# Kernel optimization log

Measured on AMD Instinct MI355X. Metric: run time of the kernel, lower is better.

## Reference

```python
import jax, jax.numpy as jnp
import numpy as np

N = 50000
E = 800000
D = 128
NEG_SLOPE = 0.2


def _gat_layer(x, W, al, ar, b, src, dst):
    """Single-head DGL-style GATConv with ReLU activation."""
    z = x @ W                                    # [N, D] projected features
    el = z @ al                                  # [N] left attention logits
    er = z @ ar                                  # [N] right attention logits
    e = jax.nn.leaky_relu(el[src] + er[dst], NEG_SLOPE)   # [E]
    # softmax over incoming edges per destination node (numerically stable)
    m = jax.ops.segment_max(e, dst, num_segments=N)       # [N]
    ex = jnp.exp(e - m[dst])                               # [E]
    s = jax.ops.segment_sum(ex, dst, num_segments=N)       # [N]
    alpha = ex / s[dst]                                    # [E]
    out = jax.ops.segment_sum(alpha[:, None] * z[src], dst, num_segments=N)  # [N, D]
    return jax.nn.relu(out + b)


def setup_inputs() -> dict:
    key = jax.random.key(0)
    ks = jax.random.split(key, 16)
    s = 0.05
    inp = {
        "f": jax.random.normal(ks[0], (N, D), dtype=jnp.float32),
        "src": jax.random.randint(ks[1], (E,), 0, N, dtype=jnp.int32),
        "dst": jax.random.randint(ks[2], (E,), 0, N, dtype=jnp.int32),
    }
    for i, kb in zip((1, 2, 3), (3, 7, 11)):
        inp[f"W{i}"] = jax.random.normal(ks[kb], (D, D), dtype=jnp.float32) * s
        inp[f"al{i}"] = jax.random.normal(ks[kb + 1], (D,), dtype=jnp.float32) * s
        inp[f"ar{i}"] = jax.random.normal(ks[kb + 2], (D,), dtype=jnp.float32) * s
        inp[f"b{i}"] = jnp.zeros((D,), dtype=jnp.float32)
    return inp


def reference(f, src, dst, W1, al1, ar1, b1, W2, al2, ar2, b2, W3, al3, ar3, b3):
    h = _gat_layer(f, W1, al1, ar1, b1, src, dst)
    h = _gat_layer(h, W2, al2, ar2, b2, src, dst)
    h = _gat_layer(h, W3, al3, ar3, b3, src, dst)
    return h  # [N, D] (single head already squeezed)
```

## Files before the change

kernel.cpp:

```cpp
#include <hip/hip_runtime.h>
#include <hip/hip_fp16.h>
#include <math.h>

#define NN 50000
#define NE 800000
#define DD 128
#define NEG_SLOPE 0.2f
#define CAP 64
#define GBLK ((NN + 127) / 128)
#define WSBLK (3 * 16384 / 256)
#define HBLK ((NE + 255) / 256)
#define SBLK ((NE + 511) / 512)

typedef short frag8 __attribute__((ext_vector_type(8)));
typedef float f32x4 __attribute__((ext_vector_type(4)));

__device__ __forceinline__ unsigned bf16_rne(float x) {
  unsigned u = __float_as_uint(x);
  return (u + 0x7FFFu + ((u >> 16) & 1u)) >> 16;
}

__device__ __forceinline__ void wsplit_body(
    int bid, const float* __restrict__ W0, const float* __restrict__ W1,
    const float* __restrict__ W2, short* __restrict__ Wh, short* __restrict__ Wl) {
  int gidx = bid * 256 + threadIdx.x;
  int L = gidx >> 14;
  int idx = gidx & 16383;
  const float* W = (L == 0) ? W0 : (L == 1) ? W1 : W2;
  int j = idx & 7;
  int lane = (idx >> 3) & 63;
  int tile = idx >> 9;
  int nt = tile & 7, kt = tile >> 3;
  int k = kt * 32 + (lane >> 4) * 8 + j;
  int n = nt * 16 + (lane & 15);
  float x = W[k * DD + n];
  unsigned hu = bf16_rne(x);
  float hf = __uint_as_float(hu << 16);
  unsigned lu = bf16_rne(x - hf);
  Wh[gidx] = (short)hu;
  Wl[gidx] = (short)lu;
}

__device__ __forceinline__ void hist_body(int bid, const int* __restrict__ dst,
                                          int* __restrict__ deg,
                                          unsigned short* __restrict__ edge_slot) {
  int i = bid * 256 + threadIdx.x;
  if (i < NE) edge_slot[i] = (unsigned short)atomicAdd(&deg[dst[i]], 1);
}

__global__ __launch_bounds__(256) void fused_pre(
    const float* __restrict__ W0, const float* __restrict__ W1, const float* __restrict__ W2,
    short* __restrict__ Wh, short* __restrict__ Wl,
    const int* __restrict__ dst, int* __restrict__ deg,
    unsigned short* __restrict__ edge_slot) {
  if (blockIdx.x < WSBLK) wsplit_body(blockIdx.x, W0, W1, W2, Wh, Wl);
  else hist_body(blockIdx.x - WSBLK, dst, deg, edge_slot);
}

__device__ __forceinline__ void gemm_body(
    int bid, short (*sB)[8192],
    const float* __restrict__ x, const short* __restrict__ Wh, const short* __restrict__ Wl,
    const float* __restrict__ al, const float* __restrict__ ar,
    __half* __restrict__ z, float* __restrict__ el, float* __restrict__ er) {
  const int t = threadIdx.x;
  const int w = t >> 6, lane = t & 63;
  const int m = lane & 15, quad = lane >> 4;
  const int R0 = bid * 128 + w * 16;

  auto stage = [&](int kt, int buf) {
    const uint4* gh = (const uint4*)(Wh + kt * 4096);
    const uint4* gl = (const uint4*)(Wl + kt * 4096);
    uint4* s = (uint4*)sB[buf];
    s[t] = gh[t];
    s[t + 512] = gl[t];
  };

  f32x4 acc[8];
#pragma unroll
  for (int nt = 0; nt < 8; nt++) acc[nt] = (f32x4)(0.f);

  int rA = R0 + m; if (rA > NN - 1) rA = NN - 1;

  stage(0, 0);
  __syncthreads();

#pragma unroll
  for (int kt = 0; kt < 4; kt++) {
    const int buf = kt & 1;
    if (kt < 3) stage(kt + 1, buf ^ 1);

    const float* xp = x + (size_t)rA * DD + kt * 32 + quad * 8;
    float xv[8];
    *(float4*)(xv) = *(const float4*)xp;
    *(float4*)(xv + 4) = *(const float4*)(xp + 4);
    frag8 ah, alo;
#pragma unroll
    for (int j = 0; j < 8; j++) {
      unsigned hu = bf16_rne(xv[j]);
      float hf = __uint_as_float(hu << 16);
      ah[j] = (short)hu;
      alo[j] = (short)bf16_rne(xv[j] - hf);
    }
#pragma unroll
    for (int nt = 0; nt < 8; nt++) {
      frag8 bh = *(const frag8*)&sB[buf][nt * 512 + lane * 8];
      frag8 bl = *(const frag8*)&sB[buf][4096 + nt * 512 + lane * 8];
      acc[nt] = __builtin_amdgcn_mfma_f32_16x16x32_bf16(alo, bh, acc[nt], 0, 0, 0);
      acc[nt] = __builtin_amdgcn_mfma_f32_16x16x32_bf16(ah, bl, acc[nt], 0, 0, 0);
      acc[nt] = __builtin_amdgcn_mfma_f32_16x16x32_bf16(ah, bh, acc[nt], 0, 0, 0);
    }
    __syncthreads();
  }

  float alv[8], arv[8];
#pragma unroll
  for (int nt = 0; nt < 8; nt++) { alv[nt] = al[nt * 16 + m]; arv[nt] = ar[nt * 16 + m]; }
#pragma unroll
  for (int r = 0; r < 4; r++) {
    float pl = 0.f, pr = 0.f;
#pragma unroll
    for (int nt = 0; nt < 8; nt++) { pl += acc[nt][r] * alv[nt]; pr += acc[nt][r] * arv[nt]; }
#pragma unroll
    for (int off = 8; off; off >>= 1) {
      pl += __shfl_xor(pl, off, 64);
      pr += __shfl_xor(pr, off, 64);
    }
    int row = R0 + quad * 4 + r;
    if (row < NN) {
      if (m == 0) { el[row] = pl; er[row] = pr; }
#pragma unroll
      for (int nt = 0; nt < 8; nt++) {
        unsigned short hu = __half_as_ushort(__float2half(acc[nt][r]));
        unsigned short hn = (unsigned short)__shfl_xor((int)hu, 1, 64);
        if ((m & 1) == 0) {
          __half2 pair = __halves2half2(__ushort_as_half(hu), __ushort_as_half(hn));
          *(__half2*)(z + (size_t)row * DD + nt * 16 + m) = pair;
        }
      }
    }
  }
}

__device__ __forceinline__ void scatter_body(
    int bid, const int* __restrict__ src, const int* __restrict__ dst,
    const unsigned short* __restrict__ edge_slot, unsigned short* __restrict__ csr_src) {
  int i = bid * 512 + threadIdx.x;
  if (i >= NE) return;
  int slot = edge_slot[i]; if (slot > CAP - 1) slot = CAP - 1;
  csr_src[dst[i] * CAP + slot] = (unsigned short)src[i];
}

__global__ __launch_bounds__(512) void gemm_mfma(
    const float* __restrict__ x, const short* __restrict__ Wh, const short* __restrict__ Wl,
    const float* __restrict__ al, const float* __restrict__ ar,
    __half* __restrict__ z, float* __restrict__ el, float* __restrict__ er) {
  __shared__ __align__(16) short sB[2][8192];
  gemm_body(blockIdx.x, sB, x, Wh, Wl, al, ar, z, el, er);
}

__global__ __launch_bounds__(512) void fused_scatter_gemm(
    const float* __restrict__ x, const short* __restrict__ Wh, const short* __restrict__ Wl,
    const float* __restrict__ al, const float* __restrict__ ar,
    __half* __restrict__ z, float* __restrict__ el, float* __restrict__ er,
    const int* __restrict__ src, const int* __restrict__ dst,
    const unsigned short* __restrict__ edge_slot, unsigned short* __restrict__ csr_src) {
  __shared__ __align__(16) short sB[2][8192];
  if (blockIdx.x < GBLK) gemm_body(blockIdx.x, sB, x, Wh, Wl, al, ar, z, el, er);
  else scatter_body(blockIdx.x - GBLK, src, dst, edge_slot, csr_src);
}

__global__ __launch_bounds__(256) void gat_agg(
    const int* __restrict__ deg, const unsigned short* __restrict__ csr_src,
    const float* __restrict__ el, const float* __restrict__ er,
    const __half* __restrict__ z, const float* __restrict__ b,
    float* __restrict__ out) {
  int node = (int)((blockIdx.x * 256 + threadIdx.x) >> 6);
  int lane = threadIdx.x & 63;
  if (node >= NN) return;
  int dn = deg[node]; if (dn > CAP) dn = CAP;
  int beg = node * CAP, end = beg + dn;
  float erd = er[node];
  const __half2* zb = (const __half2*)z + lane;

  float2 acc = make_float2(0.f, 0.f);
  float ssum = 0.f;
  for (int base = beg; base < end; base += 64) {
    int j = base + lane;
    int sn = 0; float w = 0.f;
    if (j < end) {
      sn = csr_src[j];
      float e = el[sn] + erd;
      e = (e > 0.f) ? e : NEG_SLOPE * e;
      w = __expf(e);
    }
    ssum += w;
    int cnt = min(64, end - base);
    int jj = 0;
    for (; jj + 8 <= cnt; jj += 8) {
      float ww[8]; int ss[8];
#pragma unroll
      for (int u = 0; u < 8; u++) {
        ww[u] = __shfl(w, jj + u, 64);
        ss[u] = __shfl(sn, jj + u, 64);
      }
      float2 zv[8];
#pragma unroll
      for (int u = 0; u < 8; u++) zv[u] = __half22float2(zb[(size_t)ss[u] * 64]);
#pragma unroll
      for (int u = 0; u < 8; u++) { acc.x += ww[u] * zv[u].x; acc.y += ww[u] * zv[u].y; }
    }
    for (; jj < cnt; jj++) {
      float wj = __shfl(w, jj, 64);
      int snj = __shfl(sn, jj, 64);
      float2 zv = __half22float2(zb[(size_t)snj * 64]);
      acc.x += wj * zv.x; acc.y += wj * zv.y;
    }
  }
#pragma unroll
  for (int off = 32; off; off >>= 1) ssum += __shfl_xor(ssum, off, 64);
  float inv_s = (dn > 0) ? 1.f / ssum : 0.f;

  float2 bv = *(const float2*)(b + lane * 2);
  float ox = fmaxf(acc.x * inv_s + bv.x, 0.f);
  float oy = fmaxf(acc.y * inv_s + bv.y, 0.f);
  *(float2*)(out + (size_t)node * DD + lane * 2) = make_float2(ox, oy);
}

extern "C" void kernel_launch(void* const* d_in, const int* in_sizes, int n_in,
                              void* d_out, int out_size, void* d_ws, size_t ws_size,
                              hipStream_t stream) {
  const float* f   = (const float*)d_in[0];
  const int*   src = (const int*)d_in[1];
  const int*   dst = (const int*)d_in[2];
  const float* W[3]  = {(const float*)d_in[3], (const float*)d_in[7],  (const float*)d_in[11]};
  const float* al[3] = {(const float*)d_in[4], (const float*)d_in[8],  (const float*)d_in[12]};
  const float* ar[3] = {(const float*)d_in[5], (const float*)d_in[9],  (const float*)d_in[13]};
  const float* bb[3] = {(const float*)d_in[6], (const float*)d_in[10], (const float*)d_in[14]};

  short* Wh3 = (short*)d_ws;
  short* Wl3 = Wh3 + 3 * 16384;
  __half* zbuf = (__half*)(Wl3 + 3 * 16384);
  float* hbuf = (float*)(zbuf + (size_t)NN * DD);
  float* el = hbuf + (size_t)NN * DD;
  float* er = el + NN;
  int* deg = (int*)(er + NN);
  unsigned short* edge_slot = (unsigned short*)(deg + NN);
  unsigned short* csr_src   = edge_slot + NE;

  hipMemsetAsync(deg, 0, NN * sizeof(int), stream);
  fused_pre<<<WSBLK + HBLK, 256, 0, stream>>>(W[0], W[1], W[2], Wh3, Wl3, dst, deg, edge_slot);
  fused_scatter_gemm<<<GBLK + SBLK, 512, 0, stream>>>(f, Wh3, Wl3, al[0], ar[0],
                                                      zbuf, el, er,
                                                      src, dst, edge_slot, csr_src);
  gat_agg<<<(NN * 64) / 256, 256, 0, stream>>>(deg, csr_src, el, er, zbuf, bb[0], hbuf);

  gemm_mfma<<<GBLK, 512, 0, stream>>>(hbuf, Wh3 + 16384, Wl3 + 16384,
                                      al[1], ar[1], zbuf, el, er);
  gat_agg<<<(NN * 64) / 256, 256, 0, stream>>>(deg, csr_src, el, er, zbuf, bb[1], hbuf);

  gemm_mfma<<<GBLK, 512, 0, stream>>>(hbuf, Wh3 + 2 * 16384, Wl3 + 2 * 16384,
                                      al[2], ar[2], zbuf, el, er);
  gat_agg<<<(NN * 64) / 256, 256, 0, stream>>>(deg, csr_src, el, er, zbuf, bb[2],
                                               (float*)d_out);
}
```

Baseline: 287.0 us.

## Fuse aggregation with next-layer GEMM and merge histogram with CSR scatter

Layer 1 and 2 aggregation now happen inside a new agg_gemm kernel that keeps the aggregated 32-row tile in shared memory and feeds it straight into the MFMA projection for the next layer. This removes the fp32 hidden-state round trip through global memory and two kernel launches. The degree histogram and CSR scatter are merged into one pass that uses the atomic slot directly, so the edge_slot buffer and its extra read are gone. Trade-offs: z and el/er are double-buffered, agg_gemm runs the gather with 512-thread blocks under launch bounds of 6 waves per EU, and the histogram no longer overlaps with the weight split.

```diff
diff --git a/kernel.cpp b/kernel.cpp
--- a/kernel.cpp
+++ b/kernel.cpp
@@ -9,8 +9,8 @@
 #define CAP 64
 #define GBLK ((NN + 127) / 128)
 #define WSBLK (3 * 16384 / 256)
-#define HBLK ((NE + 255) / 256)
-#define SBLK ((NE + 511) / 512)
+#define HSBLK ((NE + 511) / 512)
+#define AGBLK ((NN + 31) / 32)
 
 typedef short frag8 __attribute__((ext_vector_type(8)));
 typedef float f32x4 __attribute__((ext_vector_type(4)));
@@ -20,10 +20,10 @@
   return (u + 0x7FFFu + ((u >> 16) & 1u)) >> 16;
 }
 
-__device__ __forceinline__ void wsplit_body(
-    int bid, const float* __restrict__ W0, const float* __restrict__ W1,
+__global__ __launch_bounds__(256) void wsplit(
+    const float* __restrict__ W0, const float* __restrict__ W1,
     const float* __restrict__ W2, short* __restrict__ Wh, short* __restrict__ Wl) {
-  int gidx = bid * 256 + threadIdx.x;
+  int gidx = blockIdx.x * 256 + threadIdx.x;
   int L = gidx >> 14;
   int idx = gidx & 16383;
   const float* W = (L == 0) ? W0 : (L == 1) ? W1 : W2;
@@ -41,20 +41,15 @@
   Wl[gidx] = (short)lu;
 }
 
-__device__ __forceinline__ void hist_body(int bid, const int* __restrict__ dst,
-                                          int* __restrict__ deg,
-                                          unsigned short* __restrict__ edge_slot) {
-  int i = bid * 256 + threadIdx.x;
-  if (i < NE) edge_slot[i] = (unsigned short)atomicAdd(&deg[dst[i]], 1);
-}
-
-__global__ __launch_bounds__(256) void fused_pre(
-    const float* __restrict__ W0, const float* __restrict__ W1, const float* __restrict__ W2,
-    short* __restrict__ Wh, short* __restrict__ Wl,
-    const int* __restrict__ dst, int* __restrict__ deg,
-    unsigned short* __restrict__ edge_slot) {
-  if (blockIdx.x < WSBLK) wsplit_body(blockIdx.x, W0, W1, W2, Wh, Wl);
-  else hist_body(blockIdx.x - WSBLK, dst, deg, edge_slot);
+__device__ __forceinline__ void histscatter_body(
+    int bid, const int* __restrict__ src, const int* __restrict__ dst,
+    int* __restrict__ deg, unsigned short* __restrict__ csr_src) {
+  int i = bid * 512 + threadIdx.x;
+  if (i >= NE) return;
+  int d = dst[i];
+  int slot = atomicAdd(&deg[d], 1);
+  if (slot > CAP - 1) slot = CAP - 1;
+  csr_src[d * CAP + slot] = (unsigned short)src[i];
 }
 
 __device__ __forceinline__ void gemm_body(
@@ -141,45 +136,23 @@
   }
 }
 
-__device__ __forceinline__ void scatter_body(
-    int bid, const int* __restrict__ src, const int* __restrict__ dst,
-    const unsigned short* __restrict__ edge_slot, unsigned short* __restrict__ csr_src) {
-  int i = bid * 512 + threadIdx.x;
-  if (i >= NE) return;
-  int slot = edge_slot[i]; if (slot > CAP - 1) slot = CAP - 1;
-  csr_src[dst[i] * CAP + slot] = (unsigned short)src[i];
-}
-
-__global__ __launch_bounds__(512) void gemm_mfma(
-    const float* __restrict__ x, const short* __restrict__ Wh, const short* __restrict__ Wl,
-    const float* __restrict__ al, const float* __restrict__ ar,
-    __half* __restrict__ z, float* __restrict__ el, float* __restrict__ er) {
-  __shared__ __align__(16) short sB[2][8192];
-  gemm_body(blockIdx.x, sB, x, Wh, Wl, al, ar, z, el, er);
-}
-
-__global__ __launch_bounds__(512) void fused_scatter_gemm(
+__global__ __launch_bounds__(512) void fused_gemm_scatter(
     const float* __restrict__ x, const short* __restrict__ Wh, const short* __restrict__ Wl,
     const float* __restrict__ al, const float* __restrict__ ar,
     __half* __restrict__ z, float* __restrict__ el, float* __restrict__ er,
     const int* __restrict__ src, const int* __restrict__ dst,
-    const unsigned short* __restrict__ edge_slot, unsigned short* __restrict__ csr_src) {
+    int* __restrict__ deg, unsigned short* __restrict__ csr_src) {
   __shared__ __align__(16) short sB[2][8192];
   if (blockIdx.x < GBLK) gemm_body(blockIdx.x, sB, x, Wh, Wl, al, ar, z, el, er);
-  else scatter_body(blockIdx.x - GBLK, src, dst, edge_slot, csr_src);
-}
-
-__global__ __launch_bounds__(256) void gat_agg(
-    const int* __restrict__ deg, const unsigned short* __restrict__ csr_src,
-    const float* __restrict__ el, const float* __restrict__ er,
-    const __half* __restrict__ z, const float* __restrict__ b,
-    float* __restrict__ out) {
-  int node = (int)((blockIdx.x * 256 + threadIdx.x) >> 6);
-  int lane = threadIdx.x & 63;
-  if (node >= NN) return;
+  else histscatter_body(blockIdx.x - GBLK, src, dst, deg, csr_src);
+}
+
+__device__ __forceinline__ float2 agg_node(
+    int node, int lane, const int* __restrict__ deg,
+    const unsigned short* __restrict__ csr_src, const float* __restrict__ el,
+    float erd, const __half* __restrict__ z, float* inv_s_out) {
   int dn = deg[node]; if (dn > CAP) dn = CAP;
   int beg = node * CAP, end = beg + dn;
-  float erd = er[node];
   const __half2* zb = (const __half2*)z + lane;
 
   float2 acc = make_float2(0.f, 0.f);
@@ -218,11 +191,136 @@
   }
 #pragma unroll
   for (int off = 32; off; off >>= 1) ssum += __shfl_xor(ssum, off, 64);
-  float inv_s = (dn > 0) ? 1.f / ssum : 0.f;
-
-  float2 bv = *(const float2*)(b + lane * 2);
-  float ox = fmaxf(acc.x * inv_s + bv.x, 0.f);
-  float oy = fmaxf(acc.y * inv_s + bv.y, 0.f);
+  *inv_s_out = (dn > 0) ? 1.f / ssum : 0.f;
+  return acc;
+}
+
+__global__ __launch_bounds__(512, 6) void agg_gemm(
+    const int* __restrict__ deg, const unsigned short* __restrict__ csr_src,
+    const float* __restrict__ el_in, const float* __restrict__ er_in,
+    const __half* __restrict__ z_in, const float* __restrict__ bias,
+    const short* __restrict__ Wh, const short* __restrict__ Wl,
+    const float* __restrict__ al, const float* __restrict__ ar,
+    __half* __restrict__ z_out, float* __restrict__ el_out, float* __restrict__ er_out) {
+  __shared__ __align__(16) float hS[32][132];
+  __shared__ __align__(16) short sB[2][8192];
+  __shared__ float elp[4][32], erp[4][32];
+
+  const int t = threadIdx.x;
+  const int w = t >> 6, lane = t & 63;
+  const int R0 = blockIdx.x * 32;
+
+  auto stage = [&](int kt, int buf) {
+    const uint4* gh = (const uint4*)(Wh + kt * 4096);
+    const uint4* gl = (const uint4*)(Wl + kt * 4096);
+    uint4* s = (uint4*)sB[buf];
+    s[t] = gh[t];
+    s[t + 512] = gl[t];
+  };
+
+  stage(0, 0);
+
+  float2 bv = *(const float2*)(bias + lane * 2);
+#pragma unroll 1
+  for (int u = 0; u < 4; u++) {
+    int lrow = w * 4 + u;
+    int node = R0 + lrow;
+    float hx = 0.f, hy = 0.f;
+    if (node < NN) {
+      float inv_s;
+      float2 acc = agg_node(node, lane, deg, csr_src, el_in, er_in[node], z_in, &inv_s);
+      hx = fmaxf(acc.x * inv_s + bv.x, 0.f);
+      hy = fmaxf(acc.y * inv_s + bv.y, 0.f);
+    }
+    *(float2*)&hS[lrow][lane * 2] = make_float2(hx, hy);
+  }
+  __syncthreads();
+
+  const int m = lane & 15, quad = lane >> 4;
+  const int mt = w >> 2, p = w & 3;
+  const int nt0 = p, nt1 = p + 4;
+  f32x4 acc0 = (f32x4)(0.f), acc1 = (f32x4)(0.f);
+
+#pragma unroll
+  for (int kt = 0; kt < 4; kt++) {
+    const int buf = kt & 1;
+    if (kt < 3) stage(kt + 1, buf ^ 1);
+
+    const float* hp = &hS[mt * 16 + m][kt * 32 + quad * 8];
+    float xv[8];
+    *(float4*)(xv) = *(const float4*)hp;
+    *(float4*)(xv + 4) = *(const float4*)(hp + 4);
+    frag8 ah, alo;
+#pragma unroll
+    for (int j = 0; j < 8; j++) {
+      unsigned hu = bf16_rne(xv[j]);
+      float hf = __uint_as_float(hu << 16);
+      ah[j] = (short)hu;
+      alo[j] = (short)bf16_rne(xv[j] - hf);
+    }
+    frag8 bh0 = *(const frag8*)&sB[buf][nt0 * 512 + lane * 8];
+    frag8 bl0 = *(const frag8*)&sB[buf][4096 + nt0 * 512 + lane * 8];
+    frag8 bh1 = *(const frag8*)&sB[buf][nt1 * 512 + lane * 8];
+    frag8 bl1 = *(const frag8*)&sB[buf][4096 + nt1 * 512 + lane * 8];
+    acc0 = __builtin_amdgcn_mfma_f32_16x16x32_bf16(alo, bh0, acc0, 0, 0, 0);
+    acc0 = __builtin_amdgcn_mfma_f32_16x16x32_bf16(ah, bl0, acc0, 0, 0, 0);
+    acc0 = __builtin_amdgcn_mfma_f32_16x16x32_bf16(ah, bh0, acc0, 0, 0, 0);
+    acc1 = __builtin_amdgcn_mfma_f32_16x16x32_bf16(alo, bh1, acc1, 0, 0, 0);
+    acc1 = __builtin_amdgcn_mfma_f32_16x16x32_bf16(ah, bl1, acc1, 0, 0, 0);
+    acc1 = __builtin_amdgcn_mfma_f32_16x16x32_bf16(ah, bh1, acc1, 0, 0, 0);
+    __syncthreads();
+  }
+
+  float alv0 = al[nt0 * 16 + m], arv0 = ar[nt0 * 16 + m];
+  float alv1 = al[nt1 * 16 + m], arv1 = ar[nt1 * 16 + m];
+#pragma unroll
+  for (int r = 0; r < 4; r++) {
+    float pl = acc0[r] * alv0 + acc1[r] * alv1;
+    float pr = acc0[r] * arv0 + acc1[r] * arv1;
+#pragma unroll
+    for (int off = 8; off; off >>= 1) {
+      pl += __shfl_xor(pl, off, 64);
+      pr += __shfl_xor(pr, off, 64);
+    }
+    int lrow = mt * 16 + quad * 4 + r;
+    if (m == 0) { elp[p][lrow] = pl; erp[p][lrow] = pr; }
+    int row = R0 + lrow;
+    if (row < NN) {
+      unsigned short hu0 = __half_as_ushort(__float2half(acc0[r]));
+      unsigned short hn0 = (unsigned short)__shfl_xor((int)hu0, 1, 64);
+      unsigned short hu1 = __half_as_ushort(__float2half(acc1[r]));
+      unsigned short hn1 = (unsigned short)__shfl_xor((int)hu1, 1, 64);
+      if ((m & 1) == 0) {
+        *(__half2*)(z_out + (size_t)row * DD + nt0 * 16 + m) =
+            __halves2half2(__ushort_as_half(hu0), __ushort_as_half(hn0));
+        *(__half2*)(z_out + (size_t)row * DD + nt1 * 16 + m) =
+            __halves2half2(__ushort_as_half(hu1), __ushort_as_half(hn1));
+      }
+    }
+  }
+  __syncthreads();
+  if (t < 32) {
+    int row = R0 + t;
+    if (row < NN) {
+      el_out[row] = elp[0][t] + elp[1][t] + elp[2][t] + elp[3][t];
+      er_out[row] = erp[0][t] + erp[1][t] + erp[2][t] + erp[3][t];
+    }
+  }
+}
+
+__global__ __launch_bounds__(256) void gat_agg(
+    const int* __restrict__ deg, const unsigned short* __restrict__ csr_src,
+    const float* __restrict__ el, const float* __restrict__ er,
+    const __half* __restrict__ z, const float* __restrict__ b,
+    float* __restrict__ out) {
+  int node = (int)((blockIdx.x * 256 + threadIdx.x) >> 6);
+  int lane = threadIdx.x & 63;
+  if (node >= NN) return;
+  float inv_s;
+  float2 acc = agg_node(node, lane, deg, csr_src, el, er[node], z, &inv_s);
+  float2 bvv = *(const float2*)(b + lane * 2);
+  float ox = fmaxf(acc.x * inv_s + bvv.x, 0.f);
+  float oy = fmaxf(acc.y * inv_s + bvv.y, 0.f);
   *(float2*)(out + (size_t)node * DD + lane * 2) = make_float2(ox, oy);
 }
 
@@ -239,27 +337,26 @@
 
   short* Wh3 = (short*)d_ws;
   short* Wl3 = Wh3 + 3 * 16384;
-  __half* zbuf = (__half*)(Wl3 + 3 * 16384);
-  float* hbuf = (float*)(zbuf + (size_t)NN * DD);
-  float* el = hbuf + (size_t)NN * DD;
-  float* er = el + NN;
-  int* deg = (int*)(er + NN);
-  unsigned short* edge_slot = (unsigned short*)(deg + NN);
-  unsigned short* csr_src   = edge_slot + NE;
+  __half* zA = (__half*)(Wl3 + 3 * 16384);
+  __half* zB = zA + (size_t)NN * DD;
+  float* el  = (float*)(zB + (size_t)NN * DD);
+  float* er  = el + NN;
+  float* el2 = er + NN;
+  float* er2 = el2 + NN;
+  int* deg = (int*)(er2 + NN);
+  unsigned short* csr_src = (unsigned short*)(deg + NN);
 
   hipMemsetAsync(deg, 0, NN * sizeof(int), stream);
-  fused_pre<<<WSBLK + HBLK, 256, 0, stream>>>(W[0], W[1], W[2], Wh3, Wl3, dst, deg, edge_slot);
-  fused_scatter_gemm<<<GBLK + SBLK, 512, 0, stream>>>(f, Wh3, Wl3, al[0], ar[0],
-                                                      zbuf, el, er,
-                                                      src, dst, edge_slot, csr_src);
-  gat_agg<<<(NN * 64) / 256, 256, 0, stream>>>(deg, csr_src, el, er, zbuf, bb[0], hbuf);
-
-  gemm_mfma<<<GBLK, 512, 0, stream>>>(hbuf, Wh3 + 16384, Wl3 + 16384,
-                                      al[1], ar[1], zbuf, el, er);
-  gat_agg<<<(NN * 64) / 256, 256, 0, stream>>>(deg, csr_src, el, er, zbuf, bb[1], hbuf);
-
-  gemm_mfma<<<GBLK, 512, 0, stream>>>(hbuf, Wh3 + 2 * 16384, Wl3 + 2 * 16384,
-                                      al[2], ar[2], zbuf, el, er);
-  gat_agg<<<(NN * 64) / 256, 256, 0, stream>>>(deg, csr_src, el, er, zbuf, bb[2],
+  wsplit<<<WSBLK, 256, 0, stream>>>(W[0], W[1], W[2], Wh3, Wl3);
+  fused_gemm_scatter<<<GBLK + HSBLK, 512, 0, stream>>>(f, Wh3, Wl3, al[0], ar[0],
+                                                       zA, el, er,
+                                                       src, dst, deg, csr_src);
+  agg_gemm<<<AGBLK, 512, 0, stream>>>(deg, csr_src, el, er, zA, bb[0],
+                                      Wh3 + 16384, Wl3 + 16384, al[1], ar[1],
+                                      zB, el2, er2);
+  agg_gemm<<<AGBLK, 512, 0, stream>>>(deg, csr_src, el2, er2, zB, bb[1],
+                                      Wh3 + 2 * 16384, Wl3 + 2 * 16384, al[2], ar[2],
+                                      zA, el, er);
+  gat_agg<<<(NN * 64) / 256, 256, 0, stream>>>(deg, csr_src, el, er, zA, bb[2],
                                                (float*)d_out);
 }
```

Result: slower. 330.5 us (+15.2%).

## Split GEMM N-dimension across waves and simplify single-pass aggregation loop

Applied to the files above, without the earlier changes.

The GEMM block now covers 64 rows instead of 128. The 8 waves split the 128 output columns into two halves of four tiles each, and partial attention logits are combined through shared memory. This doubles the grid and halves the accumulator registers per wave, which is meant to raise occupancy and parallelism, at the cost of an extra barrier and redundant A-fragment conversion. The aggregation kernel drops the outer 64-edge chunk loop, since degree is capped at 64, and uses a single padded 8-way unrolled loop with no scalar tail. Padded lanes read row 0 with zero weight, which adds some wasted loads.

```diff
diff --git a/kernel.cpp b/kernel.cpp
--- a/kernel.cpp
+++ b/kernel.cpp
@@ -7,7 +7,7 @@
 #define DD 128
 #define NEG_SLOPE 0.2f
 #define CAP 64
-#define GBLK ((NN + 127) / 128)
+#define GBLK ((NN + 63) / 64)
 #define WSBLK (3 * 16384 / 256)
 #define HBLK ((NE + 255) / 256)
 #define SBLK ((NE + 511) / 512)
@@ -58,14 +58,16 @@
 }
 
 __device__ __forceinline__ void gemm_body(
-    int bid, short (*sB)[8192],
+    int bid, short (*sB)[8192], float (*elp)[64], float (*erp)[64],
     const float* __restrict__ x, const short* __restrict__ Wh, const short* __restrict__ Wl,
     const float* __restrict__ al, const float* __restrict__ ar,
     __half* __restrict__ z, float* __restrict__ el, float* __restrict__ er) {
   const int t = threadIdx.x;
   const int w = t >> 6, lane = t & 63;
   const int m = lane & 15, quad = lane >> 4;
-  const int R0 = bid * 128 + w * 16;
+  const int half = w >> 2, mw = w & 3;
+  const int ntb = half * 4;
+  const int R0 = bid * 64 + mw * 16;
 
   auto stage = [&](int kt, int buf) {
     const uint4* gh = (const uint4*)(Wh + kt * 4096);
@@ -75,9 +77,9 @@
     s[t + 512] = gl[t];
   };
 
-  f32x4 acc[8];
-#pragma unroll
-  for (int nt = 0; nt < 8; nt++) acc[nt] = (f32x4)(0.f);
+  f32x4 acc[4];
+#pragma unroll
+  for (int n = 0; n < 4; n++) acc[n] = (f32x4)(0.f);
 
   int rA = R0 + m; if (rA > NN - 1) rA = NN - 1;
 
@@ -102,41 +104,53 @@
       alo[j] = (short)bf16_rne(xv[j] - hf);
     }
 #pragma unroll
-    for (int nt = 0; nt < 8; nt++) {
-      frag8 bh = *(const frag8*)&sB[buf][nt * 512 + lane * 8];
-      frag8 bl = *(const frag8*)&sB[buf][4096 + nt * 512 + lane * 8];
-      acc[nt] = __builtin_amdgcn_mfma_f32_16x16x32_bf16(alo, bh, acc[nt], 0, 0, 0);
-      acc[nt] = __builtin_amdgcn_mfma_f32_16x16x32_bf16(ah, bl, acc[nt], 0, 0, 0);
-      acc[nt] = __builtin_amdgcn_mfma_f32_16x16x32_bf16(ah, bh, acc[nt], 0, 0, 0);
+    for (int n = 0; n < 4; n++) {
+      frag8 bh = *(const frag8*)&sB[buf][(ntb + n) * 512 + lane * 8];
+      frag8 bl = *(const frag8*)&sB[buf][4096 + (ntb + n) * 512 + lane * 8];
+      acc[n] = __builtin_amdgcn_mfma_f32_16x16x32_bf16(alo, bh, acc[n], 0, 0, 0);
+      acc[n] = __builtin_amdgcn_mfma_f32_16x16x32_bf16(ah, bl, acc[n], 0, 0, 0);
+      acc[n] = __builtin_amdgcn_mfma_f32_16x16x32_bf16(ah, bh, acc[n], 0, 0, 0);
     }
     __syncthreads();
   }
 
-  float alv[8], arv[8];
-#pragma unroll
-  for (int nt = 0; nt < 8; nt++) { alv[nt] = al[nt * 16 + m]; arv[nt] = ar[nt * 16 + m]; }
+  float alv[4], arv[4];
+#pragma unroll
+  for (int n = 0; n < 4; n++) {
+    alv[n] = al[(ntb + n) * 16 + m];
+    arv[n] = ar[(ntb + n) * 16 + m];
+  }
 #pragma unroll
   for (int r = 0; r < 4; r++) {
     float pl = 0.f, pr = 0.f;
 #pragma unroll
-    for (int nt = 0; nt < 8; nt++) { pl += acc[nt][r] * alv[nt]; pr += acc[nt][r] * arv[nt]; }
+    for (int n = 0; n < 4; n++) { pl += acc[n][r] * alv[n]; pr += acc[n][r] * arv[n]; }
 #pragma unroll
     for (int off = 8; off; off >>= 1) {
       pl += __shfl_xor(pl, off, 64);
       pr += __shfl_xor(pr, off, 64);
     }
+    int lrow = mw * 16 + quad * 4 + r;
+    if (m == 0) { elp[half][lrow] = pl; erp[half][lrow] = pr; }
     int row = R0 + quad * 4 + r;
     if (row < NN) {
-      if (m == 0) { el[row] = pl; er[row] = pr; }
-#pragma unroll
-      for (int nt = 0; nt < 8; nt++) {
-        unsigned short hu = __half_as_ushort(__float2half(acc[nt][r]));
+#pragma unroll
+      for (int n = 0; n < 4; n++) {
+        unsigned short hu = __half_as_ushort(__float2half(acc[n][r]));
         unsigned short hn = (unsigned short)__shfl_xor((int)hu, 1, 64);
         if ((m & 1) == 0) {
           __half2 pair = __halves2half2(__ushort_as_half(hu), __ushort_as_half(hn));
-          *(__half2*)(z + (size_t)row * DD + nt * 16 + m) = pair;
+          *(__half2*)(z + (size_t)row * DD + (ntb + n) * 16 + m) = pair;
         }
       }
+    }
+  }
+  __syncthreads();
+  if (t < 64) {
+    int row = bid * 64 + t;
+    if (row < NN) {
+      el[row] = elp[0][t] + elp[1][t];
+      er[row] = erp[0][t] + erp[1][t];
     }
   }
 }
@@ -155,7 +169,8 @@
     const float* __restrict__ al, const float* __restrict__ ar,
     __half* __restrict__ z, float* __restrict__ el, float* __restrict__ er) {
   __shared__ __align__(16) short sB[2][8192];
-  gemm_body(blockIdx.x, sB, x, Wh, Wl, al, ar, z, el, er);
+  __shared__ float elp[2][64], erp[2][64];
+  gemm_body(blockIdx.x, sB, elp, erp, x, Wh, Wl, al, ar, z, el, er);
 }
 
 __global__ __launch_bounds__(512) void fused_scatter_gemm(
@@ -165,7 +180,8 @@
     const int* __restrict__ src, const int* __restrict__ dst,
     const unsigned short* __restrict__ edge_slot, unsigned short* __restrict__ csr_src) {
   __shared__ __align__(16) short sB[2][8192];
-  if (blockIdx.x < GBLK) gemm_body(blockIdx.x, sB, x, Wh, Wl, al, ar, z, el, er);
+  __shared__ float elp[2][64], erp[2][64];
+  if (blockIdx.x < GBLK) gemm_body(blockIdx.x, sB, elp, erp, x, Wh, Wl, al, ar, z, el, er);
   else scatter_body(blockIdx.x - GBLK, src, dst, edge_slot, csr_src);
 }
 
@@ -178,43 +194,32 @@
   int lane = threadIdx.x & 63;
   if (node >= NN) return;
   int dn = deg[node]; if (dn > CAP) dn = CAP;
-  int beg = node * CAP, end = beg + dn;
+  int beg = node * CAP;
   float erd = er[node];
   const __half2* zb = (const __half2*)z + lane;
 
+  int sn = 0; float wv = 0.f;
+  if (lane < dn) {
+    sn = csr_src[beg + lane];
+    float e = el[sn] + erd;
+    e = (e > 0.f) ? e : NEG_SLOPE * e;
+    wv = __expf(e);
+  }
+  float ssum = wv;
+
   float2 acc = make_float2(0.f, 0.f);
-  float ssum = 0.f;
-  for (int base = beg; base < end; base += 64) {
-    int j = base + lane;
-    int sn = 0; float w = 0.f;
-    if (j < end) {
-      sn = csr_src[j];
-      float e = el[sn] + erd;
-      e = (e > 0.f) ? e : NEG_SLOPE * e;
-      w = __expf(e);
-    }
-    ssum += w;
-    int cnt = min(64, end - base);
-    int jj = 0;
-    for (; jj + 8 <= cnt; jj += 8) {
-      float ww[8]; int ss[8];
-#pragma unroll
-      for (int u = 0; u < 8; u++) {
-        ww[u] = __shfl(w, jj + u, 64);
-        ss[u] = __shfl(sn, jj + u, 64);
-      }
-      float2 zv[8];
-#pragma unroll
-      for (int u = 0; u < 8; u++) zv[u] = __half22float2(zb[(size_t)ss[u] * 64]);
-#pragma unroll
-      for (int u = 0; u < 8; u++) { acc.x += ww[u] * zv[u].x; acc.y += ww[u] * zv[u].y; }
-    }
-    for (; jj < cnt; jj++) {
-      float wj = __shfl(w, jj, 64);
-      int snj = __shfl(sn, jj, 64);
-      float2 zv = __half22float2(zb[(size_t)snj * 64]);
-      acc.x += wj * zv.x; acc.y += wj * zv.y;
-    }
+  for (int jj = 0; jj < dn; jj += 8) {
+    float ww[8]; int ss[8];
+#pragma unroll
+    for (int u = 0; u < 8; u++) {
+      ww[u] = __shfl(wv, jj + u, 64);
+      ss[u] = __shfl(sn, jj + u, 64);
+    }
+    float2 zv[8];
+#pragma unroll
+    for (int u = 0; u < 8; u++) zv[u] = __half22float2(zb[(size_t)ss[u] * 64]);
+#pragma unroll
+    for (int u = 0; u < 8; u++) { acc.x += ww[u] * zv[u].x; acc.y += ww[u] * zv[u].y; }
   }
 #pragma unroll
   for (int off = 32; off; off >>= 1) ssum += __shfl_xor(ssum, off, 64);
```

Measured after the change: 290.6 us. No clear change (+1.3%).
